# Performance work log

Hardware: AMD Instinct MI355X
Metric: run time of the kernel (lower is better)

Reference implementation:

```python
import jax, jax.numpy as jnp
import numpy as np

SEQ_LEN = 32768
HID = 1024


def setup_inputs() -> dict:
    key = jax.random.key(0)
    k1, k2, k3, k4 = jax.random.split(key, 4)
    hidden = jax.random.normal(k1, (1, 1, HID), dtype=jnp.float32)
    encoder_outputs = jax.random.normal(k2, (SEQ_LEN, HID), dtype=jnp.float32)
    # nn.Linear(hidden_size, hidden_size): weight [H, H], bias [H]
    W = jax.random.normal(k3, (HID, HID), dtype=jnp.float32) * (1.0 / np.sqrt(HID))
    b = jax.random.normal(k4, (HID,), dtype=jnp.float32) * 0.01
    return {"hidden": hidden, "encoder_outputs": encoder_outputs, "W": W, "b": b}


def reference(hidden, encoder_outputs, W, b):
    # method == 'general':
    #   energy_i = Linear(enc_i) = W @ enc_i + b     -> [S, H]
    #   e_i = sum(hidden[-1, 0] * energy_i)           -> [S]
    h = hidden[-1, 0]                                 # [H]
    proj = jnp.einsum('sh,dh->sd', encoder_outputs, W) + b  # [S, H]
    energies = proj @ h                               # [S]
    attn = jax.nn.softmax(energies, axis=0)           # [S]
    return attn[None, None, :]                        # [1, 1, S]
```

## Files before the change

kernel.cpp:

```cpp
#include <hip/hip_runtime.h>
#include <hip/hip_bf16.h>
#include <math.h>

#define SEQ_LEN 32768
#define HID 1024

__global__ void __launch_bounds__(256) k_matvec(const float* __restrict__ W,
                                                const float* __restrict__ hvec,
                                                float* __restrict__ v) {
    const int col = blockIdx.x;
    const int t = threadIdx.x;
    float acc = 0.f;
#pragma unroll
    for (int i = 0; i < 4; ++i) {
        const int d = (i << 8) + t;
        acc = fmaf(hvec[d], W[d * HID + col], acc);
    }
#pragma unroll
    for (int off = 32; off; off >>= 1) acc += __shfl_xor(acc, off, 64);
    __shared__ float red[4];
    if ((t & 63) == 0) red[t >> 6] = acc;
    __syncthreads();
    if (t == 0) v[col] = (red[0] + red[1]) + (red[2] + red[3]);
}

__global__ void __launch_bounds__(256) k_energy(const float* __restrict__ enc,
                                                const float* __restrict__ v,
                                                float* __restrict__ energies,
                                                float2* __restrict__ bstats) {
    const int t = threadIdx.x;
    const int wave = t >> 6;
    const int lane = t & 63;
    const int row0 = (blockIdx.x << 5) + (wave << 3);

    const float4 vr0 = *reinterpret_cast<const float4*>(v +       (lane << 2));
    const float4 vr1 = *reinterpret_cast<const float4*>(v + 256 + (lane << 2));
    const float4 vr2 = *reinterpret_cast<const float4*>(v + 512 + (lane << 2));
    const float4 vr3 = *reinterpret_cast<const float4*>(v + 768 + (lane << 2));

    float m = -__builtin_inff();
    float z = 0.f;

    const float4* p = reinterpret_cast<const float4*>(enc + (size_t)row0 * HID) + lane;
    float4 a = p[0], b = p[64], c = p[128], d = p[192];

#pragma unroll
    for (int r = 0; r < 8; ++r) {
        float4 na, nb, nc, nd;
        if (r < 7) {
            const float4* q = p + (size_t)(r + 1) * 256;
            na = q[0]; nb = q[64]; nc = q[128]; nd = q[192];
        }
        float acc = a.x * vr0.x + a.y * vr0.y + a.z * vr0.z + a.w * vr0.w
                  + b.x * vr1.x + b.y * vr1.y + b.z * vr1.z + b.w * vr1.w
                  + c.x * vr2.x + c.y * vr2.y + c.z * vr2.z + c.w * vr2.w
                  + d.x * vr3.x + d.y * vr3.y + d.z * vr3.z + d.w * vr3.w;
#pragma unroll
        for (int off = 32; off; off >>= 1) acc += __shfl_xor(acc, off, 64);
        if (lane == 0) energies[row0 + r] = acc;
        const float nm = fmaxf(m, acc);
        z = z * __expf(m - nm) + __expf(acc - nm);
        m = nm;
        a = na; b = nb; c = nc; d = nd;
    }

    __shared__ float wm[4], wz[4];
    if (lane == 0) { wm[wave] = m; wz[wave] = z; }
    __syncthreads();
    if (t == 0) {
        float M = fmaxf(fmaxf(wm[0], wm[1]), fmaxf(wm[2], wm[3]));
        float Z = wz[0] * __expf(wm[0] - M) + wz[1] * __expf(wm[1] - M)
                + wz[2] * __expf(wm[2] - M) + wz[3] * __expf(wm[3] - M);
        bstats[blockIdx.x] = make_float2(M, Z);
    }
}

__global__ void __launch_bounds__(256) k_final(const float* __restrict__ energies,
                                               const float2* __restrict__ bstats,
                                               float* __restrict__ out) {
    __shared__ float sm[256], sz[256];
    const int t = threadIdx.x;
    float m = -__builtin_inff();
    float z = 0.f;
#pragma unroll
    for (int i = 0; i < 4; ++i) {
        const float2 s = bstats[t + (i << 8)];
        const float nm = fmaxf(m, s.x);
        z = z * __expf(m - nm) + s.y * __expf(s.x - nm);
        m = nm;
    }
    sm[t] = m; sz[t] = z;
    __syncthreads();
    for (int off = 128; off; off >>= 1) {
        if (t < off) {
            const float m1 = sm[t], z1 = sz[t];
            const float m2 = sm[t + off], z2 = sz[t + off];
            const float M = fmaxf(m1, m2);
            sm[t] = M;
            sz[t] = z1 * __expf(m1 - M) + z2 * __expf(m2 - M);
        }
        __syncthreads();
    }
    const float M = sm[0];
    const float rZ = 1.f / sz[0];

    const size_t i = ((size_t)blockIdx.x << 9) + ((size_t)t << 1);
    const float2 e = *reinterpret_cast<const float2*>(energies + i);
    float2 o;
    o.x = __expf(e.x - M) * rZ;
    o.y = __expf(e.y - M) * rZ;
    *reinterpret_cast<float2*>(out + i) = o;
}

extern "C" void kernel_launch(void* const* d_in, const int* in_sizes, int n_in,
                              void* d_out, int out_size, void* d_ws, size_t ws_size,
                              hipStream_t stream) {
    const float* hidden = (const float*)d_in[0];
    const float* enc    = (const float*)d_in[1];
    const float* W      = (const float*)d_in[2];

    float* ws       = (float*)d_ws;
    float* v        = ws;
    float* energies = ws + HID;
    float2* bstats  = (float2*)(ws + HID + SEQ_LEN);

    k_matvec<<<HID, 256, 0, stream>>>(W, hidden, v);
    k_energy<<<SEQ_LEN / 32, 256, 0, stream>>>(enc, v, energies, bstats);
    k_final<<<SEQ_LEN / 512, 256, 0, stream>>>(energies, bstats, (float*)d_out);
}
```

Before: 37.00 us.

## Fuse softmax finalize into energy kernel via atomic last-block election

Drops the separate normalization kernel. Each block publishes its energies and running max/sum with atomics. A two-level counter elects the last 32 finishing groups as finisher blocks; one of them reduces the global stats and raises a flag the others spin on, and then each finisher normalizes a 1024-element slice. This removes a kernel launch and its gap, but adds atomic traffic, spinning on a flag, and only 32 blocks doing the output pass. Global control counters are reset by the last departing block.

After: 38.79 us. 4.8% more time.

```diff
diff --git a/kernel.cpp b/kernel.cpp
--- a/kernel.cpp
+++ b/kernel.cpp
@@ -1,9 +1,34 @@
 #include <hip/hip_runtime.h>
-#include <hip/hip_bf16.h>
 #include <math.h>
 
-#define SEQ_LEN 32768
 #define HID 1024
+#define NBLK 1024
+#define RLX __ATOMIC_RELAXED
+#define AGT __HIP_MEMORY_SCOPE_AGENT
+
+__device__ unsigned g_ctl[1152];
+#define SUB(g)   ((g) << 5)
+#define MASTER   1024
+#define FLAG     1056
+#define DEPART   1088
+
+__device__ __forceinline__ unsigned ld32(const unsigned* p) { return __hip_atomic_load(p, RLX, AGT); }
+__device__ __forceinline__ void st32(unsigned* p, unsigned v) { __hip_atomic_store(p, v, RLX, AGT); }
+__device__ __forceinline__ unsigned long long ld64(const unsigned long long* p) { return __hip_atomic_load(p, RLX, AGT); }
+__device__ __forceinline__ void st64(unsigned long long* p, unsigned long long v) { __hip_atomic_store(p, v, RLX, AGT); }
+__device__ __forceinline__ unsigned add32(unsigned* p, unsigned v) { return __hip_atomic_fetch_add(p, v, RLX, AGT); }
+__device__ __forceinline__ void vfence() { asm volatile("s_waitcnt vmcnt(0)" ::: "memory"); }
+__device__ __forceinline__ void spin(unsigned* f) {
+    for (int i = 0; i < (1 << 24); ++i) {
+        if (ld32(f)) return;
+        __builtin_amdgcn_s_sleep(2);
+    }
+}
+__device__ __forceinline__ void mzmerge(float& m, float& z, float m2, float z2) {
+    const float M = fmaxf(m, m2);
+    z = z * __expf(m - M) + z2 * __expf(m2 - M);
+    m = M;
+}
 
 __global__ void __launch_bounds__(256) k_matvec(const float* __restrict__ W,
                                                 const float* __restrict__ hvec,
@@ -24,92 +49,119 @@
     if (t == 0) v[col] = (red[0] + red[1]) + (red[2] + red[3]);
 }
 
-__global__ void __launch_bounds__(256) k_energy(const float* __restrict__ enc,
-                                                const float* __restrict__ v,
-                                                float* __restrict__ energies,
-                                                float2* __restrict__ bstats) {
-    const int t = threadIdx.x;
-    const int wave = t >> 6;
-    const int lane = t & 63;
-    const int row0 = (blockIdx.x << 5) + (wave << 3);
+__global__ void __launch_bounds__(256)
+k_energy(const float* __restrict__ enc, const float* __restrict__ v,
+         unsigned* __restrict__ eglob, unsigned long long* __restrict__ bstats,
+         unsigned long long* __restrict__ fstat, float* __restrict__ out) {
+    const int t = threadIdx.x, bid = blockIdx.x;
+    const int wave = t >> 6, lane = t & 63;
 
-    const float4 vr0 = *reinterpret_cast<const float4*>(v +       (lane << 2));
-    const float4 vr1 = *reinterpret_cast<const float4*>(v + 256 + (lane << 2));
-    const float4 vr2 = *reinterpret_cast<const float4*>(v + 512 + (lane << 2));
-    const float4 vr3 = *reinterpret_cast<const float4*>(v + 768 + (lane << 2));
+    __shared__ float wm[4], wz[4];
+    __shared__ float e_lds[32];
+    __shared__ float sm[256], sz[256];
+    __shared__ int s_role;
+    __shared__ float2 s_mz;
 
-    float m = -__builtin_inff();
-    float z = 0.f;
+    {
+        const int row0 = (bid << 5) + (wave << 3);
+        const float4 vr0 = *reinterpret_cast<const float4*>(v +       (lane << 2));
+        const float4 vr1 = *reinterpret_cast<const float4*>(v + 256 + (lane << 2));
+        const float4 vr2 = *reinterpret_cast<const float4*>(v + 512 + (lane << 2));
+        const float4 vr3 = *reinterpret_cast<const float4*>(v + 768 + (lane << 2));
 
-    const float4* p = reinterpret_cast<const float4*>(enc + (size_t)row0 * HID) + lane;
-    float4 a = p[0], b = p[64], c = p[128], d = p[192];
+        float m = -__builtin_inff();
+        float z = 0.f;
+
+        const float4* p = reinterpret_cast<const float4*>(enc + (size_t)row0 * HID) + lane;
+        float4 a = p[0], b = p[64], c = p[128], d = p[192];
 
 #pragma unroll
-    for (int r = 0; r < 8; ++r) {
-        float4 na, nb, nc, nd;
-        if (r < 7) {
-            const float4* q = p + (size_t)(r + 1) * 256;
-            na = q[0]; nb = q[64]; nc = q[128]; nd = q[192];
+        for (int r = 0; r < 8; ++r) {
+            float4 na, nb, nc, nd;
+            if (r < 7) {
+                const float4* q = p + (size_t)(r + 1) * 256;
+                na = q[0]; nb = q[64]; nc = q[128]; nd = q[192];
+            }
+            float acc = a.x * vr0.x + a.y * vr0.y + a.z * vr0.z + a.w * vr0.w
+                      + b.x * vr1.x + b.y * vr1.y + b.z * vr1.z + b.w * vr1.w
+                      + c.x * vr2.x + c.y * vr2.y + c.z * vr2.z + c.w * vr2.w
+                      + d.x * vr3.x + d.y * vr3.y + d.z * vr3.z + d.w * vr3.w;
+#pragma unroll
+            for (int off = 32; off; off >>= 1) acc += __shfl_xor(acc, off, 64);
+            if (!lane) e_lds[(wave << 3) + r] = acc;
+            mzmerge(m, z, acc, 1.f);
+            a = na; b = nb; c = nc; d = nd;
         }
-        float acc = a.x * vr0.x + a.y * vr0.y + a.z * vr0.z + a.w * vr0.w
-                  + b.x * vr1.x + b.y * vr1.y + b.z * vr1.z + b.w * vr1.w
-                  + c.x * vr2.x + c.y * vr2.y + c.z * vr2.z + c.w * vr2.w
-                  + d.x * vr3.x + d.y * vr3.y + d.z * vr3.z + d.w * vr3.w;
+        if (!lane) { wm[wave] = m; wz[wave] = z; }
+    }
+    __syncthreads();
+
+    if (t < 32) st32(eglob + (bid << 5) + t, __float_as_uint(e_lds[t]));
+    if (t == 0) {
+        float M = wm[0], Z = wz[0];
+        mzmerge(M, Z, wm[1], wz[1]);
+        mzmerge(M, Z, wm[2], wz[2]);
+        mzmerge(M, Z, wm[3], wz[3]);
+        st64(bstats + bid, __builtin_bit_cast(unsigned long long, make_float2(M, Z)));
+        vfence();
+        int role = -1;
+        if (add32(g_ctl + SUB(bid >> 5), 1u) == 31u)
+            role = (int)add32(g_ctl + MASTER, 1u);
+        s_role = role;
+    }
+    __syncthreads();
+    const int role = s_role;
+    if (role < 0) return;
+
+    if (role == 31) {
+        float m = -__builtin_inff(), z = 0.f;
 #pragma unroll
-        for (int off = 32; off; off >>= 1) acc += __shfl_xor(acc, off, 64);
-        if (lane == 0) energies[row0 + r] = acc;
-        const float nm = fmaxf(m, acc);
-        z = z * __expf(m - nm) + __expf(acc - nm);
-        m = nm;
-        a = na; b = nb; c = nc; d = nd;
+        for (int i = 0; i < 4; ++i) {
+            const unsigned long long bits = ld64(bstats + t + (i << 8));
+            const float2 s = __builtin_bit_cast(float2, bits);
+            mzmerge(m, z, s.x, s.y);
+        }
+        sm[t] = m; sz[t] = z;
+        __syncthreads();
+        for (int off = 128; off; off >>= 1) {
+            if (t < off) {
+                float m1 = sm[t], z1 = sz[t];
+                mzmerge(m1, z1, sm[t + off], sz[t + off]);
+                sm[t] = m1; sz[t] = z1;
+            }
+            __syncthreads();
+        }
+        if (t == 0) {
+            st64(fstat, __builtin_bit_cast(unsigned long long, make_float2(sm[0], sz[0])));
+            vfence();
+            st32(g_ctl + FLAG, 1u);
+        }
+    } else {
+        if (t == 0) spin(g_ctl + FLAG);
+    }
+    __syncthreads();
+    if (t == 0) s_mz = __builtin_bit_cast(float2, ld64(fstat));
+    __syncthreads();
+
+    const float M = s_mz.x;
+    const float rZ = 1.f / s_mz.y;
+    const int base = role << 10;
+#pragma unroll
+    for (int i = 0; i < 4; ++i) {
+        const int r = base + (i << 8) + t;
+        const float e = __uint_as_float(ld32(eglob + r));
+        out[r] = __expf(e - M) * rZ;
     }
 
-    __shared__ float wm[4], wz[4];
-    if (lane == 0) { wm[wave] = m; wz[wave] = z; }
-    __syncthreads();
     if (t == 0) {
-        float M = fmaxf(fmaxf(wm[0], wm[1]), fmaxf(wm[2], wm[3]));
-        float Z = wz[0] * __expf(wm[0] - M) + wz[1] * __expf(wm[1] - M)
-                + wz[2] * __expf(wm[2] - M) + wz[3] * __expf(wm[3] - M);
-        bstats[blockIdx.x] = make_float2(M, Z);
+        if (add32(g_ctl + DEPART, 1u) == 31u) {
+#pragma unroll
+            for (int g = 0; g < 32; ++g) st32(g_ctl + SUB(g), 0u);
+            st32(g_ctl + MASTER, 0u);
+            st32(g_ctl + FLAG, 0u);
+            st32(g_ctl + DEPART, 0u);
+        }
     }
-}
-
-__global__ void __launch_bounds__(256) k_final(const float* __restrict__ energies,
-                                               const float2* __restrict__ bstats,
-                                               float* __restrict__ out) {
-    __shared__ float sm[256], sz[256];
-    const int t = threadIdx.x;
-    float m = -__builtin_inff();
-    float z = 0.f;
-#pragma unroll
-    for (int i = 0; i < 4; ++i) {
-        const float2 s = bstats[t + (i << 8)];
-        const float nm = fmaxf(m, s.x);
-        z = z * __expf(m - nm) + s.y * __expf(s.x - nm);
-        m = nm;
-    }
-    sm[t] = m; sz[t] = z;
-    __syncthreads();
-    for (int off = 128; off; off >>= 1) {
-        if (t < off) {
-            const float m1 = sm[t], z1 = sz[t];
-            const float m2 = sm[t + off], z2 = sz[t + off];
-            const float M = fmaxf(m1, m2);
-            sm[t] = M;
-            sz[t] = z1 * __expf(m1 - M) + z2 * __expf(m2 - M);
-        }
-        __syncthreads();
-    }
-    const float M = sm[0];
-    const float rZ = 1.f / sz[0];
-
-    const size_t i = ((size_t)blockIdx.x << 9) + ((size_t)t << 1);
-    const float2 e = *reinterpret_cast<const float2*>(energies + i);
-    float2 o;
-    o.x = __expf(e.x - M) * rZ;
-    o.y = __expf(e.y - M) * rZ;
-    *reinterpret_cast<float2*>(out + i) = o;
 }
 
 extern "C" void kernel_launch(void* const* d_in, const int* in_sizes, int n_in,
@@ -119,12 +171,12 @@
     const float* enc    = (const float*)d_in[1];
     const float* W      = (const float*)d_in[2];
 
-    float* ws       = (float*)d_ws;
+    float* ws = (float*)d_ws;
     float* v        = ws;
-    float* energies = ws + HID;
-    float2* bstats  = (float2*)(ws + HID + SEQ_LEN);
+    unsigned* eglob = (unsigned*)(ws + HID);
+    unsigned long long* bstats = (unsigned long long*)(ws + HID + 32768);
+    unsigned long long* fstat  = bstats + 1024;
 
     k_matvec<<<HID, 256, 0, stream>>>(W, hidden, v);
-    k_energy<<<SEQ_LEN / 32, 256, 0, stream>>>(enc, v, energies, bstats);
-    k_final<<<SEQ_LEN / 512, 256, 0, stream>>>(energies, bstats, (float*)d_out);
+    k_energy<<<NBLK, 256, 0, stream>>>(enc, v, eglob, bstats, fstat, (float*)d_out);
 }
```
